# Optimization experiments

Measured on AMD Instinct MI355X. Metric: run time of the kernel, lower is better.

## Reference

```python
import jax, jax.numpy as jnp
import numpy as np

IN_DIM, OUT_DIM = 4096, 11008
NUM_SUBDIM, KS = 1376, 256
DS = OUT_DIM // NUM_SUBDIM  # 8
BATCH = 32


def setup_inputs() -> dict:
    key = jax.random.key(0)
    k1, k2, k3, k4 = jax.random.split(key, 4)
    x = jax.random.normal(k1, (BATCH, IN_DIM), dtype=jnp.float32)
    vectors = jax.random.normal(k2, (NUM_SUBDIM, KS, DS), dtype=jnp.float32)
    bias = jax.random.normal(k3, (OUT_DIM,), dtype=jnp.float32)
    indexes = jax.random.randint(k4, (IN_DIM, NUM_SUBDIM), 0, KS, dtype=jnp.int64)
    return {"x": x, "vectors": vectors, "bias": bias, "indexes": indexes}


def reference(x, vectors, bias, indexes):
    in_dim, num_subdim = indexes.shape
    ds = vectors.shape[-1]
    # PQ dequant: gather codewords per (row, subspace) -> [in_dim, num_subdim, Ds]
    # vectors[d, indexes[i, d]] via broadcast of arange(num_subdim) against indexes.
    dims = jnp.arange(num_subdim)
    weight = vectors[dims, indexes].reshape(in_dim, num_subdim * ds)  # [in_dim, out_dim]
    return x @ weight + bias
```

## Files before the change

kernel.cpp:

```cpp
#include <hip/hip_runtime.h>

#define IN_DIM  4096
#define OUT_DIM 11008
#define NSUB    1376
#define KSQ     256
#define DSUB    8
#define BATCH   32

#define DTILE   8
#define NTILE   64
#define KC      64
#define KSPLIT  16
#define KPB     (IN_DIM / KSPLIT)
#define NCHUNK  (KPB / KC)
#define NBLK    (OUT_DIM / NTILE)
#define NBLKP   176
#define GRID_MAIN (NBLKP * KSPLIT)

typedef unsigned short ushort_t;
typedef unsigned int   uint_t;
typedef unsigned char  uchar_t;
typedef __attribute__((ext_vector_type(8))) short bf16x8;
typedef __attribute__((ext_vector_type(4))) float f32x4;

#define VEC_N    (NSUB * KSQ * DSUB)
#define XBF_OFF  (VEC_N * 2)
#define IDXT_OFF (XBF_OFF + BATCH * IN_DIM * 2)
#define SLAB_OFF (IDXT_OFF + NSUB * IN_DIM)
#define PREP_V   (VEC_N / 2)
#define PREP_X   (BATCH * IN_DIM / 2)
#define PREP_N   (PREP_V + PREP_X)
#define PACK_BLK (PREP_N / 256)
#define IDXT_BLK ((IN_DIM / 128) * (NSUB / 32))

__device__ __forceinline__ ushort_t f2bf(float f) {
    union { float f; uint_t u; } a; a.f = f;
    uint_t u = a.u;
    u += 0x7fffu + ((u >> 16) & 1u);
    return (ushort_t)(u >> 16);
}

__global__ __launch_bounds__(256) void pq_prep(
    const float* __restrict__ x, const float* __restrict__ vecs,
    const int* __restrict__ idx,
    uint_t* __restrict__ vbf, uint_t* __restrict__ xbf,
    uchar_t* __restrict__ idx8T)
{
    __shared__ uchar_t sT[32][144];
    const int t = threadIdx.x;

    if (blockIdx.x < PACK_BLK) {
        int tid = blockIdx.x * 256 + t;
        if (tid < PREP_V) {
            float2 v = ((const float2*)vecs)[tid];
            vbf[tid] = (uint_t)f2bf(v.x) | ((uint_t)f2bf(v.y) << 16);
        } else {
            int i = tid - PREP_V;
            float2 v = ((const float2*)x)[i];
            xbf[i] = (uint_t)f2bf(v.x) | ((uint_t)f2bf(v.y) << 16);
        }
        return;
    }

    const int bid = blockIdx.x - PACK_BLK;
    const int k0 = (bid & 31) * 128, d0 = (bid >> 5) * 32;
    #pragma unroll
    for (int p = 0; p < 16; ++p) {
        int f = p * 256 + t;
        int kk = f >> 5, dd = f & 31;
        sT[dd][kk] = (uchar_t)idx[(size_t)(k0 + kk) * NSUB + d0 + dd];
    }
    __syncthreads();
    int dd = t >> 3, seg = t & 7;
    uint4 v = *(const uint4*)&sT[dd][seg * 16];
    *(uint4*)&idx8T[(size_t)(d0 + dd) * IN_DIM + k0 + seg * 16] = v;
}

__global__ __launch_bounds__(256, 4) void pq_main(
    const ushort_t* __restrict__ xbf, const uint4* __restrict__ vbf4,
    const uchar_t* __restrict__ idx8T, float* __restrict__ slab)
{
    __shared__ uint4  sV4[4 * 512];
    __shared__ uint_t sW32[4 * 16 * 32];

    const int id   = blockIdx.x;
    const int xcd  = id & 7;
    const int slot = id >> 3;
    const int kblk = slot & 15;
    const int nblk = (slot >> 4) * 8 + xcd;
    if (nblk >= NBLK) return;

    const int t    = threadIdx.x;
    const int w    = t >> 6;
    const int lane = t & 63;
    const int d0   = nblk * DTILE;
    const int kbase = kblk * KPB;

    const int l15 = lane & 15;
    const int l4  = lane >> 4;
    const int dl  = lane >> 5;
    const int q   = lane & 31;

    uint4 vst[8];
    const size_t src0 = (size_t)(d0 + w * 2) * KSQ;
    #pragma unroll
    for (int p = 0; p < 8; ++p)
        vst[p] = vbf4[src0 + p * 64 + lane];

    bf16x8 A[2][8];
    #pragma unroll
    for (int mt = 0; mt < 2; ++mt)
        #pragma unroll
        for (int kk = 0; kk < 8; ++kk)
            A[mt][kk] = *(const bf16x8*)
                &xbf[(size_t)(mt * 16 + l15) * IN_DIM + kbase + kk * 32 + l4 * 8];

    const uchar_t* idxrow = idx8T + (size_t)(d0 + w * 2 + dl) * IN_DIM + kbase;
    uint_t bb[NCHUNK];
    #pragma unroll
    for (int c = 0; c < NCHUNK; ++c)
        bb[c] = *(const ushort_t*)&idxrow[c * KC + q * 2];

    #pragma unroll
    for (int p = 0; p < 8; ++p)
        sV4[w * 512 + p * 64 + lane] = vst[p];

    __builtin_amdgcn_sched_barrier(0);

    f32x4 acc[2];
    acc[0] = (f32x4)0.0f; acc[1] = (f32x4)0.0f;

    const int vbase = w * 512 + dl * 256;
    const int Rbase = (w * 16 + dl * 8) * 32;

    #pragma unroll
    for (int c = 0; c < NCHUNK; ++c) {
        uint4 g0 = sV4[vbase + (bb[c] & 255)];
        uint4 g1 = sV4[vbase + (bb[c] >> 8)];

        #pragma unroll
        for (int j = 0; j < 8; ++j) {
            const uint_t sel = (j & 1) ? 0x07060302u : 0x05040100u;
            uint_t a0 = (j >> 1) == 0 ? g0.x : (j >> 1) == 1 ? g0.y : (j >> 1) == 2 ? g0.z : g0.w;
            uint_t a1 = (j >> 1) == 0 ? g1.x : (j >> 1) == 1 ? g1.y : (j >> 1) == 2 ? g1.z : g1.w;
            uint_t wv = __builtin_amdgcn_perm(a1, a0, sel);
            int dw = ((((q >> 2) ^ j) << 2) | (q & 3));
            sW32[Rbase + j * 32 + dw] = wv;
        }

        #pragma unroll
        for (int kq = 0; kq < 2; ++kq) {
            int u16 = (kq * 4 + l4) ^ (l15 & 7);
            bf16x8 B = *(const bf16x8*)
                ((const char*)sW32 + (w * 16 + l15) * 128 + u16 * 16);
            #pragma unroll
            for (int mt = 0; mt < 2; ++mt)
                acc[mt] = __builtin_amdgcn_mfma_f32_16x16x32_bf16(
                    A[mt][c * 2 + kq], B, acc[mt], 0, 0, 0);
        }
    }

    float* sl = slab + (size_t)kblk * BATCH * OUT_DIM;
    const int col = nblk * NTILE + w * 16 + l15;
    #pragma unroll
    for (int mt = 0; mt < 2; ++mt)
        #pragma unroll
        for (int r = 0; r < 4; ++r)
            sl[(size_t)(mt * 16 + l4 * 4 + r) * OUT_DIM + col] = acc[mt][r];
}

__global__ __launch_bounds__(256) void pq_reduce(
    const float* __restrict__ slab, const float* __restrict__ bias,
    float* __restrict__ out)
{
    int i = blockIdx.x * 256 + threadIdx.x;
    int m = i / (OUT_DIM / 4), n4 = i % (OUT_DIM / 4);
    float4 s = ((const float4*)bias)[n4];
    #pragma unroll
    for (int kb = 0; kb < KSPLIT; ++kb) {
        float4 v = ((const float4*)slab)[(size_t)(kb * BATCH + m) * (OUT_DIM / 4) + n4];
        s.x += v.x; s.y += v.y; s.z += v.z; s.w += v.w;
    }
    ((float4*)out)[(size_t)m * (OUT_DIM / 4) + n4] = s;
}

extern "C" void kernel_launch(void* const* d_in, const int* in_sizes, int n_in,
                              void* d_out, int out_size, void* d_ws, size_t ws_size,
                              hipStream_t stream) {
    const float* x    = (const float*)d_in[0];
    const float* vecs = (const float*)d_in[1];
    const float* bias = (const float*)d_in[2];
    const int*   idx  = (const int*)d_in[3];
    float* out = (float*)d_out;

    uint_t*  vbf   = (uint_t*)d_ws;
    uint_t*  xbf   = (uint_t*)((char*)d_ws + XBF_OFF);
    uchar_t* idx8T = (uchar_t*)((char*)d_ws + IDXT_OFF);
    float*   slab  = (float*)((char*)d_ws + SLAB_OFF);

    pq_prep<<<PACK_BLK + IDXT_BLK, 256, 0, stream>>>(x, vecs, idx, vbf, xbf, idx8T);
    pq_main<<<GRID_MAIN, 256, 0, stream>>>(
        (const ushort_t*)xbf, (const uint4*)vbf, idx8T, slab);
    pq_reduce<<<(BATCH * OUT_DIM / 4) / 256, 256, 0, stream>>>(slab, bias, out);
}
```

Measured before the change: 116.6 us.

## Halve K-split, process two K halves per block, remap blocks to XCDs

Reduces the K-split from 16 to 8 so each block covers 512 K values in two 256-wide halves. Each block stages its codebook slice in LDS once and reuses it across both halves. This halves the slab traffic and the reduction work, and also halves the number of blocks. The block-to-XCD mapping changes so that each XCD owns a contiguous range of N tiles across all K blocks, which may help L2 reuse of codebook slices. The risk is fewer blocks in flight and a more serial inner loop per block, which can lower latency hiding.

```diff
diff --git a/kernel.cpp b/kernel.cpp
--- a/kernel.cpp
+++ b/kernel.cpp
@@ -10,11 +10,12 @@
 #define DTILE   8
 #define NTILE   64
 #define KC      64
-#define KSPLIT  16
+#define KSPLIT  8
 #define KPB     (IN_DIM / KSPLIT)
-#define NCHUNK  (KPB / KC)
+#define NCHUNK  4
 #define NBLK    (OUT_DIM / NTILE)
 #define NBLKP   176
+#define NPX     (NBLKP / 8)
 #define GRID_MAIN (NBLKP * KSPLIT)
 
 typedef unsigned short ushort_t;
@@ -77,17 +78,17 @@
 }
 
 __global__ __launch_bounds__(256, 4) void pq_main(
-    const ushort_t* __restrict__ xbf, const uint4* __restrict__ vbf4,
+    const ushort_t* __restrict__ xbfu, const uint4* __restrict__ vbf4,
     const uchar_t* __restrict__ idx8T, float* __restrict__ slab)
 {
     __shared__ uint4  sV4[4 * 512];
     __shared__ uint_t sW32[4 * 16 * 32];
 
-    const int id   = blockIdx.x;
-    const int xcd  = id & 7;
-    const int slot = id >> 3;
-    const int kblk = slot & 15;
-    const int nblk = (slot >> 4) * 8 + xcd;
+    const int id  = blockIdx.x;
+    const int xcd = id & 7;
+    const int s   = id >> 3;
+    const int nblk = xcd * NPX + (s % NPX);
+    const int kblk = s / NPX;
     if (nblk >= NBLK) return;
 
     const int t    = threadIdx.x;
@@ -101,62 +102,71 @@
     const int dl  = lane >> 5;
     const int q   = lane & 31;
 
-    uint4 vst[8];
-    const size_t src0 = (size_t)(d0 + w * 2) * KSQ;
-    #pragma unroll
-    for (int p = 0; p < 8; ++p)
-        vst[p] = vbf4[src0 + p * 64 + lane];
-
-    bf16x8 A[2][8];
-    #pragma unroll
-    for (int mt = 0; mt < 2; ++mt)
-        #pragma unroll
-        for (int kk = 0; kk < 8; ++kk)
-            A[mt][kk] = *(const bf16x8*)
-                &xbf[(size_t)(mt * 16 + l15) * IN_DIM + kbase + kk * 32 + l4 * 8];
-
-    const uchar_t* idxrow = idx8T + (size_t)(d0 + w * 2 + dl) * IN_DIM + kbase;
-    uint_t bb[NCHUNK];
-    #pragma unroll
-    for (int c = 0; c < NCHUNK; ++c)
-        bb[c] = *(const ushort_t*)&idxrow[c * KC + q * 2];
-
-    #pragma unroll
-    for (int p = 0; p < 8; ++p)
-        sV4[w * 512 + p * 64 + lane] = vst[p];
-
-    __builtin_amdgcn_sched_barrier(0);
+    {
+        const size_t src0 = (size_t)(d0 + w * 2) * KSQ;
+        #pragma unroll
+        for (int h = 0; h < 2; ++h) {
+            uint4 vst[4];
+            #pragma unroll
+            for (int p = 0; p < 4; ++p)
+                vst[p] = vbf4[src0 + (h * 4 + p) * 64 + lane];
+            #pragma unroll
+            for (int p = 0; p < 4; ++p)
+                sV4[w * 512 + (h * 4 + p) * 64 + lane] = vst[p];
+        }
+    }
 
     f32x4 acc[2];
     acc[0] = (f32x4)0.0f; acc[1] = (f32x4)0.0f;
 
+    const uchar_t* idxrow = idx8T + (size_t)(d0 + w * 2 + dl) * IN_DIM + kbase;
     const int vbase = w * 512 + dl * 256;
     const int Rbase = (w * 16 + dl * 8) * 32;
 
     #pragma unroll
-    for (int c = 0; c < NCHUNK; ++c) {
-        uint4 g0 = sV4[vbase + (bb[c] & 255)];
-        uint4 g1 = sV4[vbase + (bb[c] >> 8)];
-
-        #pragma unroll
-        for (int j = 0; j < 8; ++j) {
-            const uint_t sel = (j & 1) ? 0x07060302u : 0x05040100u;
-            uint_t a0 = (j >> 1) == 0 ? g0.x : (j >> 1) == 1 ? g0.y : (j >> 1) == 2 ? g0.z : g0.w;
-            uint_t a1 = (j >> 1) == 0 ? g1.x : (j >> 1) == 1 ? g1.y : (j >> 1) == 2 ? g1.z : g1.w;
-            uint_t wv = __builtin_amdgcn_perm(a1, a0, sel);
-            int dw = ((((q >> 2) ^ j) << 2) | (q & 3));
-            sW32[Rbase + j * 32 + dw] = wv;
-        }
-
-        #pragma unroll
-        for (int kq = 0; kq < 2; ++kq) {
-            int u16 = (kq * 4 + l4) ^ (l15 & 7);
-            bf16x8 B = *(const bf16x8*)
-                ((const char*)sW32 + (w * 16 + l15) * 128 + u16 * 16);
-            #pragma unroll
-            for (int mt = 0; mt < 2; ++mt)
-                acc[mt] = __builtin_amdgcn_mfma_f32_16x16x32_bf16(
-                    A[mt][c * 2 + kq], B, acc[mt], 0, 0, 0);
+    for (int h = 0; h < 2; ++h) {
+        const int kh = kbase + h * 256;
+
+        bf16x8 A[2][8];
+        #pragma unroll
+        for (int mt = 0; mt < 2; ++mt)
+            #pragma unroll
+            for (int kk = 0; kk < 8; ++kk)
+                A[mt][kk] = *(const bf16x8*)
+                    &xbfu[(size_t)(mt * 16 + l15) * IN_DIM + kh + kk * 32 + l4 * 8];
+
+        uint_t bb[NCHUNK];
+        #pragma unroll
+        for (int c = 0; c < NCHUNK; ++c)
+            bb[c] = *(const ushort_t*)&idxrow[h * 256 + c * KC + q * 2];
+
+        __builtin_amdgcn_sched_barrier(0);
+
+        #pragma unroll
+        for (int c = 0; c < NCHUNK; ++c) {
+            uint4 g0 = sV4[vbase + (bb[c] & 255)];
+            uint4 g1 = sV4[vbase + (bb[c] >> 8)];
+
+            #pragma unroll
+            for (int j = 0; j < 8; ++j) {
+                const uint_t sel = (j & 1) ? 0x07060302u : 0x05040100u;
+                uint_t a0 = (j >> 1) == 0 ? g0.x : (j >> 1) == 1 ? g0.y : (j >> 1) == 2 ? g0.z : g0.w;
+                uint_t a1 = (j >> 1) == 0 ? g1.x : (j >> 1) == 1 ? g1.y : (j >> 1) == 2 ? g1.z : g1.w;
+                uint_t wv = __builtin_amdgcn_perm(a1, a0, sel);
+                int dw = ((((q >> 2) ^ j) << 2) | (q & 3));
+                sW32[Rbase + j * 32 + dw] = wv;
+            }
+
+            #pragma unroll
+            for (int kq = 0; kq < 2; ++kq) {
+                int u16 = (kq * 4 + l4) ^ (l15 & 7);
+                bf16x8 B = *(const bf16x8*)
+                    ((const char*)sW32 + (w * 16 + l15) * 128 + u16 * 16);
+                #pragma unroll
+                for (int mt = 0; mt < 2; ++mt)
+                    acc[mt] = __builtin_amdgcn_mfma_f32_16x16x32_bf16(
+                        A[mt][c * 2 + kq], B, acc[mt], 0, 0, 0);
+            }
         }
     }
 
@@ -174,7 +184,7 @@
     float* __restrict__ out)
 {
     int i = blockIdx.x * 256 + threadIdx.x;
-    int m = i / (OUT_DIM / 4), n4 = i % (OUT_DIM / 4);
+    int m = i / (OUT_DIM / 4), n4 = i - m * (OUT_DIM / 4);
     float4 s = ((const float4*)bias)[n4];
     #pragma unroll
     for (int kb = 0; kb < KSPLIT; ++kb) {
```

Measured after the change: 113.2 us. 3.0% less time.
